# Performance work log

Hardware: AMD Instinct MI355X
Metric: run time of the kernel (lower is better)

Reference implementation:

```python
import jax, jax.numpy as jnp
import numpy as np

NUM_SAMPLED = 512       # num_sampled_points
EXTRA_WIDTH = 1.0       # pool_extra_width


def setup_inputs() -> dict:
    key = jax.random.key(0)
    k1, k2, k3, k4, k5, k6 = jax.random.split(key, 6)
    B, N, C, M = 4, 16384, 128, 128
    # lidar-like points: xy in [0,40] m, z in [-2,2] m
    xy = jax.random.uniform(k1, (B, N, 2), jnp.float32, 0.0, 40.0)
    z = jax.random.uniform(k2, (B, N, 1), jnp.float32, -2.0, 2.0)
    points = jnp.concatenate([xy, z], axis=-1)
    point_features = jax.random.normal(k3, (B, N, C), jnp.float32)
    # boxes: centers in same range, dims 1-5 m, heading in [-pi, pi]
    cxy = jax.random.uniform(k4, (B, M, 2), jnp.float32, 0.0, 40.0)
    cz = jax.random.uniform(k5, (B, M, 1), jnp.float32, -1.0, 1.0)
    dims = jax.random.uniform(k6, (B, M, 3), jnp.float32, 1.0, 5.0)
    heading = jax.random.uniform(jax.random.fold_in(key, 7), (B, M, 1), jnp.float32, -3.14159, 3.14159)
    boxes3d = jnp.concatenate([cxy, cz, dims, heading], axis=-1)
    return {"points": points, "point_features": point_features, "boxes3d": boxes3d}


def _pool_one(points, feats, boxes):
    # points (N,3), feats (N,C), boxes (M,7)
    N = points.shape[0]
    center = boxes[:, 0:3]                      # (M,3)
    dims = boxes[:, 3:6] + 2.0 * EXTRA_WIDTH    # enlarge_box3d: dx,dy,dz += 2*extra
    heading = boxes[:, 6]                       # (M,)
    # shift into box-centered frame: (M,N)
    sx = points[None, :, 0] - center[:, 0:1]
    sy = points[None, :, 1] - center[:, 1:2]
    sz = points[None, :, 2] - center[:, 2:3]
    ch = jnp.cos(heading)[:, None]
    sh = jnp.sin(heading)[:, None]
    # rotate by -heading into box local frame
    lx = sx * ch + sy * sh
    ly = -sx * sh + sy * ch
    mask = (jnp.abs(lx) < dims[:, 0:1] * 0.5) \
         & (jnp.abs(ly) < dims[:, 1:2] * 0.5) \
         & (jnp.abs(sz) < dims[:, 2:3] * 0.5)   # (M,N)
    cnt = mask.sum(axis=1)                       # (M,) points in each box
    # stable order of matched point indices: matched first, in original order
    order_key = jnp.where(mask, jnp.arange(N, dtype=jnp.int32)[None, :], N)
    idx_sorted = jnp.argsort(order_key, axis=1)[:, :NUM_SAMPLED]  # (M,S)
    # slot k takes the (k mod cnt)-th matched point (wrap-around duplication)
    k = jnp.arange(NUM_SAMPLED, dtype=jnp.int32)[None, :]
    cnt_safe = jnp.maximum(cnt, 1)[:, None]
    wrapped = k % cnt_safe                       # (M,S), k when cnt>k
    gather_idx = jnp.take_along_axis(idx_sorted, wrapped, axis=1)  # (M,S)
    data = jnp.concatenate([points, feats], axis=1)  # (N,3+C)
    pooled = data[gather_idx]                    # (M,S,3+C)
    empty = (cnt == 0).astype(jnp.int32)         # (M,)
    pooled = jnp.where(empty[:, None, None] > 0, jnp.zeros((), pooled.dtype), pooled)
    return pooled, empty


def reference(points, point_features, boxes3d):
    pooled_features, pooled_empty_flag = jax.vmap(_pool_one)(points, point_features, boxes3d)
    return pooled_features, pooled_empty_flag
```

## Files before the change

### kernel.cpp

```cpp
#include <hip/hip_runtime.h>

#define BATCH 4
#define NPTS 16384
#define NBOX 128
#define NFEAT 128
#define NS 512
#define ROW 131
#define NWORDS (NPTS / 64)
#define QCHUNK 4096
#define ROWS_PER_BLK 32
#define SUBS (NS / ROWS_PER_BLK)

__global__ __launch_bounds__(256) void ballot_kernel(
    const float* __restrict__ points,
    const float* __restrict__ boxes,
    unsigned long long* __restrict__ bits_ws)
{
#pragma clang fp contract(off)
    const int blk    = blockIdx.x;
    const int box_id = blk >> 2;
    const int q      = blk & 3;
    const int b      = box_id >> 7;
    const int tid    = threadIdx.x;
    const int wave   = tid >> 6;
    const int lane   = tid & 63;

    const float* bx = boxes + box_id * 7;
    const float cx = bx[0], cy = bx[1], cz = bx[2];
    const float hx = bx[3] * 0.5f + 1.0f;
    const float hy = bx[4] * 0.5f + 1.0f;
    const float hz = bx[5] * 0.5f + 1.0f;
    const double hd = (double)bx[6];
    const float ch = (float)cos(hd);
    const float sh = (float)sin(hd);

    const float* pts = points + (size_t)b * NPTS * 3;
    unsigned long long* bw = bits_ws + (size_t)box_id * NWORDS + q * (QCHUNK / 64);

    #pragma unroll 4
    for (int it = 0; it < QCHUNK / 256; ++it) {
        const int i = q * QCHUNK + it * 256 + wave * 64 + lane;
        const float px = pts[i * 3 + 0];
        const float py = pts[i * 3 + 1];
        const float pz = pts[i * 3 + 2];
        const float sx = px - cx;
        const float sy = py - cy;
        const float sz = pz - cz;
        const float t0 = sx * ch;
        const float t1 = sy * sh;
        const float lx = t0 + t1;
        const float t2 = (-sx) * sh;
        const float t3 = sy * ch;
        const float ly = t2 + t3;
        const bool inside = (fabsf(lx) < hx) && (fabsf(ly) < hy) && (fabsf(sz) < hz);
        const unsigned long long m = __ballot(inside);
        if (lane == 0) bw[it * 4 + wave] = m;
    }
}

__global__ __launch_bounds__(256) void pool_kernel(
    const float* __restrict__ points,
    const float* __restrict__ feats,
    const unsigned long long* __restrict__ bits_ws,
    float* __restrict__ out_pooled,
    float* __restrict__ out_flag)
{
    const int blk    = blockIdx.x;
    const int box_id = blk >> 4;
    const int sub    = blk & (SUBS - 1);
    const int b      = box_id >> 7;
    const int tid    = threadIdx.x;
    const int wave   = tid >> 6;
    const int lane   = tid & 63;

    __shared__ int s_idx[NS];
    __shared__ int s_gi[ROWS_PER_BLK];
    __shared__ int s_wsum[4];
    __shared__ float s_row[ROWS_PER_BLK * ROW];

    const unsigned long long w = bits_ws[(size_t)box_id * NWORDS + tid];
    const int pc = __popcll(w);
    int pre = pc;
    #pragma unroll
    for (int off = 1; off < 64; off <<= 1) {
        const int v = __shfl_up(pre, off);
        if (lane >= off) pre += v;
    }
    if (lane == 63) s_wsum[wave] = pre;
    __syncthreads();
    int wbase = 0;
    for (int i = 0; i < wave; ++i) wbase += s_wsum[i];
    const int total = s_wsum[0] + s_wsum[1] + s_wsum[2] + s_wsum[3];
    int pos = wbase + (pre - pc);
    unsigned long long mm = w;
    while (mm && pos < NS) {
        const int bit = __builtin_ctzll(mm);
        s_idx[pos] = tid * 64 + bit;
        ++pos;
        mm &= (mm - 1);
    }
    const int cnt = (total < NS) ? total : NS;
    __syncthreads();

    if (sub == 0 && tid == 0) out_flag[box_id] = (cnt == 0) ? 1.0f : 0.0f;

    float* outg = out_pooled + (size_t)blk * (ROWS_PER_BLK * ROW);

    if (cnt == 0) {
        float4 z = make_float4(0.f, 0.f, 0.f, 0.f);
        float4* og = (float4*)outg;
        for (int i = tid; i < (ROWS_PER_BLK * ROW) / 4; i += 256) og[i] = z;
        return;
    }

    if (tid < ROWS_PER_BLK) {
        const int k = sub * ROWS_PER_BLK + tid;
        const int j = (k < cnt) ? k : (k % cnt);
        s_gi[tid] = s_idx[j];
    }
    __syncthreads();

    const float* pts = points + (size_t)b * NPTS * 3;
    const float* fb  = feats  + (size_t)b * NPTS * NFEAT;

    const int cg = lane & 31;
    const int rh = lane >> 5;
    #pragma unroll
    for (int it = 0; it < 4; ++it) {
        const int row = wave * 8 + it * 2 + rh;
        const int gi  = s_gi[row];
        const float4 f = *(const float4*)(fb + (size_t)gi * NFEAT + cg * 4);
        float* sr = s_row + row * ROW;
        sr[3 + cg * 4 + 0] = f.x;
        sr[3 + cg * 4 + 1] = f.y;
        sr[3 + cg * 4 + 2] = f.z;
        sr[3 + cg * 4 + 3] = f.w;
        if (cg < 3) sr[cg] = pts[gi * 3 + cg];
    }
    __syncthreads();

    const float4* sv = (const float4*)s_row;
    float4* og = (float4*)outg;
    for (int i = tid; i < (ROWS_PER_BLK * ROW) / 4; i += 256) og[i] = sv[i];
}

extern "C" void kernel_launch(void* const* d_in, const int* in_sizes, int n_in,
                              void* d_out, int out_size, void* d_ws, size_t ws_size,
                              hipStream_t stream) {
    const float* points = (const float*)d_in[0];
    const float* feats  = (const float*)d_in[1];
    const float* boxes  = (const float*)d_in[2];
    float* out_pooled = (float*)d_out;
    float* out_flag   = out_pooled + (size_t)BATCH * NBOX * NS * ROW;

    unsigned long long* bits_ws = (unsigned long long*)d_ws;

    ballot_kernel<<<BATCH * NBOX * 4, 256, 0, stream>>>(points, boxes, bits_ws);
    pool_kernel<<<BATCH * NBOX * SUBS, 256, 0, stream>>>(points, feats, bits_ws,
                                                         out_pooled, out_flag);
}
```

Baseline: 191.4 us.

## Move compaction into mask kernel, write gather indices, use nontemporal stores

The box-membership kernel now runs one block per box, keeps the ballot bits in shared memory and does the prefix-sum compaction once per box, writing the final 512 wrapped gather indices to workspace. The gather kernel no longer redoes the 256-word scan and compaction for each of its 16 sub-blocks; it only reads 32 indices. Output stores switch to nontemporal stores. The cost is fewer blocks (512 instead of 2048) for the mask pass, so each block now does four times the serial work with less parallelism.

Measured after the change: 215.3 us. 12.5% more time.

```diff
diff --git a/kernel.cpp b/kernel.cpp
--- a/kernel.cpp
+++ b/kernel.cpp
@@ -7,23 +7,27 @@
 #define NS 512
 #define ROW 131
 #define NWORDS (NPTS / 64)
-#define QCHUNK 4096
 #define ROWS_PER_BLK 32
 #define SUBS (NS / ROWS_PER_BLK)
 
-__global__ __launch_bounds__(256) void ballot_kernel(
+typedef float v4f __attribute__((ext_vector_type(4)));
+
+__global__ __launch_bounds__(256) void mask_compact_kernel(
     const float* __restrict__ points,
     const float* __restrict__ boxes,
-    unsigned long long* __restrict__ bits_ws)
+    int* __restrict__ gidx_ws,
+    float* __restrict__ out_flag)
 {
 #pragma clang fp contract(off)
-    const int blk    = blockIdx.x;
-    const int box_id = blk >> 2;
-    const int q      = blk & 3;
+    const int box_id = blockIdx.x;
     const int b      = box_id >> 7;
     const int tid    = threadIdx.x;
     const int wave   = tid >> 6;
     const int lane   = tid & 63;
+
+    __shared__ unsigned long long s_bits[NWORDS];
+    __shared__ int s_idx[NS];
+    __shared__ int s_wsum[4];
 
     const float* bx = boxes + box_id * 7;
     const float cx = bx[0], cy = bx[1], cz = bx[2];
@@ -35,11 +39,11 @@
     const float sh = (float)sin(hd);
 
     const float* pts = points + (size_t)b * NPTS * 3;
-    unsigned long long* bw = bits_ws + (size_t)box_id * NWORDS + q * (QCHUNK / 64);
 
     #pragma unroll 4
-    for (int it = 0; it < QCHUNK / 256; ++it) {
-        const int i = q * QCHUNK + it * 256 + wave * 64 + lane;
+    for (int it = 0; it < 64; ++it) {
+        const int word = wave * 64 + it;
+        const int i    = word * 64 + lane;
         const float px = pts[i * 3 + 0];
         const float py = pts[i * 3 + 1];
         const float pz = pts[i * 3 + 2];
@@ -54,31 +58,11 @@
         const float ly = t2 + t3;
         const bool inside = (fabsf(lx) < hx) && (fabsf(ly) < hy) && (fabsf(sz) < hz);
         const unsigned long long m = __ballot(inside);
-        if (lane == 0) bw[it * 4 + wave] = m;
+        if (lane == 0) s_bits[word] = m;
     }
-}
+    __syncthreads();
 
-__global__ __launch_bounds__(256) void pool_kernel(
-    const float* __restrict__ points,
-    const float* __restrict__ feats,
-    const unsigned long long* __restrict__ bits_ws,
-    float* __restrict__ out_pooled,
-    float* __restrict__ out_flag)
-{
-    const int blk    = blockIdx.x;
-    const int box_id = blk >> 4;
-    const int sub    = blk & (SUBS - 1);
-    const int b      = box_id >> 7;
-    const int tid    = threadIdx.x;
-    const int wave   = tid >> 6;
-    const int lane   = tid & 63;
-
-    __shared__ int s_idx[NS];
-    __shared__ int s_gi[ROWS_PER_BLK];
-    __shared__ int s_wsum[4];
-    __shared__ float s_row[ROWS_PER_BLK * ROW];
-
-    const unsigned long long w = bits_ws[(size_t)box_id * NWORDS + tid];
+    const unsigned long long w = s_bits[tid];
     const int pc = __popcll(w);
     int pre = pc;
     #pragma unroll
@@ -102,23 +86,54 @@
     const int cnt = (total < NS) ? total : NS;
     __syncthreads();
 
-    if (sub == 0 && tid == 0) out_flag[box_id] = (cnt == 0) ? 1.0f : 0.0f;
+    if (tid == 0) out_flag[box_id] = (cnt == 0) ? 1.0f : 0.0f;
+
+    int* gi = gidx_ws + (size_t)box_id * NS;
+    if (cnt == 0) {
+        gi[tid]       = -1;
+        gi[tid + 256] = -1;
+        return;
+    }
+    {
+        int k = tid;
+        int j = (k < cnt) ? k : (k % cnt);
+        gi[k] = s_idx[j];
+        k = tid + 256;
+        j = (k < cnt) ? k : (k % cnt);
+        gi[k] = s_idx[j];
+    }
+}
+
+__global__ __launch_bounds__(256) void gather_kernel(
+    const float* __restrict__ points,
+    const float* __restrict__ feats,
+    const int*   __restrict__ gidx_ws,
+    float* __restrict__ out_pooled)
+{
+    const int blk    = blockIdx.x;
+    const int box_id = blk >> 4;
+    const int sub    = blk & (SUBS - 1);
+    const int b      = box_id >> 7;
+    const int tid    = threadIdx.x;
+    const int wave   = tid >> 6;
+    const int lane   = tid & 63;
+
+    __shared__ int s_gi[ROWS_PER_BLK];
+    __shared__ float s_row[ROWS_PER_BLK * ROW];
+
+    if (tid < ROWS_PER_BLK)
+        s_gi[tid] = gidx_ws[(size_t)box_id * NS + sub * ROWS_PER_BLK + tid];
+    __syncthreads();
 
     float* outg = out_pooled + (size_t)blk * (ROWS_PER_BLK * ROW);
 
-    if (cnt == 0) {
-        float4 z = make_float4(0.f, 0.f, 0.f, 0.f);
-        float4* og = (float4*)outg;
-        for (int i = tid; i < (ROWS_PER_BLK * ROW) / 4; i += 256) og[i] = z;
+    if (s_gi[0] < 0) {
+        const v4f z = (v4f)(0.0f);
+        v4f* og = (v4f*)outg;
+        for (int i = tid; i < (ROWS_PER_BLK * ROW) / 4; i += 256)
+            __builtin_nontemporal_store(z, og + i);
         return;
     }
-
-    if (tid < ROWS_PER_BLK) {
-        const int k = sub * ROWS_PER_BLK + tid;
-        const int j = (k < cnt) ? k : (k % cnt);
-        s_gi[tid] = s_idx[j];
-    }
-    __syncthreads();
 
     const float* pts = points + (size_t)b * NPTS * 3;
     const float* fb  = feats  + (size_t)b * NPTS * NFEAT;
@@ -139,9 +154,10 @@
     }
     __syncthreads();
 
-    const float4* sv = (const float4*)s_row;
-    float4* og = (float4*)outg;
-    for (int i = tid; i < (ROWS_PER_BLK * ROW) / 4; i += 256) og[i] = sv[i];
+    const v4f* sv = (const v4f*)s_row;
+    v4f* og = (v4f*)outg;
+    for (int i = tid; i < (ROWS_PER_BLK * ROW) / 4; i += 256)
+        __builtin_nontemporal_store(sv[i], og + i);
 }
 
 extern "C" void kernel_launch(void* const* d_in, const int* in_sizes, int n_in,
@@ -153,9 +169,10 @@
     float* out_pooled = (float*)d_out;
     float* out_flag   = out_pooled + (size_t)BATCH * NBOX * NS * ROW;
 
-    unsigned long long* bits_ws = (unsigned long long*)d_ws;
+    int* gidx_ws = (int*)d_ws;
 
-    ballot_kernel<<<BATCH * NBOX * 4, 256, 0, stream>>>(points, boxes, bits_ws);
-    pool_kernel<<<BATCH * NBOX * SUBS, 256, 0, stream>>>(points, feats, bits_ws,
-                                                         out_pooled, out_flag);
+    mask_compact_kernel<<<BATCH * NBOX, 256, 0, stream>>>(points, boxes,
+                                                          gidx_ws, out_flag);
+    gather_kernel<<<BATCH * NBOX * SUBS, 256, 0, stream>>>(points, feats, gidx_ws,
+                                                           out_pooled);
 }
```
